# Kernel tuning notes

Hardware: AMD Instinct MI355X
Metric: run time of the kernel (lower is better)

The kernel has to match this reference:

```python
import jax, jax.numpy as jnp
import numpy as np

B, S, D = 2, 2048, 1024
H = 16            # attention heads
KVH = 4           # key/value heads
G = H // KVH      # group_size = 4
HD = D // H       # head_dim = 64
ROPE_THETA = 10000.0


def rope(x):
    # x: [B, S, D]; interleaved-pair rotary embedding over full last dim
    d = x.shape[-1]
    inv_freq = 1.0 / (ROPE_THETA ** (jnp.arange(0, d, 2, dtype=jnp.float32) / d))  # [d/2]
    ang = jnp.arange(x.shape[1], dtype=jnp.float32)[:, None] * inv_freq[None, :]   # [S, d/2]
    cos, sin = jnp.cos(ang), jnp.sin(ang)
    x1, x2 = x[..., 0::2], x[..., 1::2]
    r1 = x1 * cos - x2 * sin
    r2 = x1 * sin + x2 * cos
    out = jnp.stack([r1, r2], axis=-1).reshape(x.shape)
    return out


def setup_inputs() -> dict:
    key = jax.random.key(0)
    kx, kq, kk, kv = jax.random.split(key, 4)
    x = jax.random.normal(kx, (B, S, D), dtype=jnp.float32)
    # mark last 256 positions of batch element 1 as padding via NaN
    x = x.at[1, S - 256:, :].set(jnp.nan)
    scale = 1.0 / np.sqrt(D)
    Wq = jax.random.normal(kq, (D, D), dtype=jnp.float32) * scale
    Wk = jax.random.normal(kk, (D, D // G), dtype=jnp.float32) * scale
    Wv = jax.random.normal(kv, (D, D // G), dtype=jnp.float32) * scale
    return {"x": x, "Wq": Wq, "Wk": Wk, "Wv": Wv}


def reference(x, Wq, Wk, Wv):
    pad = jnp.isnan(x)                      # [B,S,D]
    x = jnp.where(pad, 0.0, x)
    key_pad = jnp.any(pad, axis=-1)         # [B,S] True = padded token

    q = x @ Wq                              # [B,S,D]
    k = jnp.repeat(x @ Wk, G, axis=-1)      # grouped KV, repeat_interleave -> [B,S,D]
    v = jnp.repeat(x @ Wv, G, axis=-1)

    q = rope(q)
    k = rope(k)

    def split_heads(t):
        return t.reshape(B, S, H, HD).transpose(0, 2, 1, 3)  # [B,H,S,HD]

    q, k, v = split_heads(q), split_heads(k), split_heads(v)

    scores = jnp.einsum('bhqd,bhkd->bhqk', q, k) / np.sqrt(HD)
    causal = jnp.tril(jnp.ones((S, S), dtype=bool))
    allow = causal[None, None, :, :] & (~key_pad)[:, None, None, :]
    scores = jnp.where(allow, scores, -1e9)
    attn = jax.nn.softmax(scores, axis=-1)
    out = jnp.einsum('bhqk,bhkd->bhqd', attn, v)
    return out.transpose(0, 2, 1, 3).reshape(B, S, D)
```

## Files before the change

kernel.cpp:

```cpp
#include <hip/hip_runtime.h>
#include <hip/hip_bf16.h>
#include <math.h>

typedef unsigned short u16;
typedef unsigned int u32;
typedef __bf16 bf16x8 __attribute__((ext_vector_type(8)));
typedef float fx4 __attribute__((ext_vector_type(4)));

#define MFMA16(a, b, c) __builtin_amdgcn_mfma_f32_16x16x32_bf16(a, b, c, 0, 0, 0)

static constexpr int Bb = 2, Ss = 2048, Dd = 1024, Hh = 16, DKV = 256;
static constexpr int NQKV = 1536;
static constexpr int ROWS = Bb * Ss;
static constexpr float L2T_OVER = 0.0259525632f;
static constexpr float SC2 = 0.18033688f;
static constexpr int PSTR = 76;
static constexpr int NUNITS = 2560;

__device__ __forceinline__ u16 f2bf(float f) {
    union { float f; u32 i; } v; v.f = f;
    u32 u = v.i;
    return (u16)((u + 0x7FFFu + ((u >> 16) & 1u)) >> 16);
}
__device__ __forceinline__ u16 bfr(float f) {
    return (u16)((__float_as_uint(f) + 0x8000u) >> 16);
}

__device__ __forceinline__ float fexp2(float x) {
    float r; asm("v_exp_f32 %0, %1" : "=v"(r) : "v"(x)); return r;
}
__device__ __forceinline__ void fsincos(float a, float& sn, float& cs) {
    float r = a * 0.15915494309189535f;
    r = r - floorf(r);
    asm("v_sin_f32 %0, %1" : "=v"(sn) : "v"(r));
    asm("v_cos_f32 %0, %1" : "=v"(cs) : "v"(r));
}

__device__ __forceinline__ void gl16(const u16* g, u16* l) {
    __builtin_amdgcn_global_load_lds(
        (const __attribute__((address_space(1))) void*)g,
        (__attribute__((address_space(3))) void*)l, 16, 0, 0);
}

template <int CTRL>
__device__ __forceinline__ float dppf(float x) {
    return __int_as_float(
        __builtin_amdgcn_mov_dpp(__float_as_int(x), CTRL, 0xF, 0xF, true));
}
__device__ __forceinline__ float rsum16(float x) {
    x += dppf<0xB1>(x);
    x += dppf<0x4E>(x);
    x += dppf<0x124>(x);
    x += dppf<0x128>(x);
    return x;
}

__global__ void pre_kernel(const float* __restrict__ x, const float* __restrict__ Wq,
                           const float* __restrict__ Wk, const float* __restrict__ Wv,
                           u16* __restrict__ xc, u32* __restrict__ kpb,
                           u16* __restrict__ wAll) {
    __shared__ u16 tile[32][33];
    __shared__ int flag;
    int bid = blockIdx.x, t = threadIdx.x;
    if (bid < 4096) {
        int row = bid;
        if (t == 0) flag = 0;
        __syncthreads();
        float4 d = *(const float4*)(x + (size_t)row * Dd + t * 4);
        int any = 0;
        float a0 = d.x, a1 = d.y, a2 = d.z, a3 = d.w;
        if ((__float_as_uint(a0) & 0x7FFFFFFFu) > 0x7F800000u) { a0 = 0.f; any = 1; }
        if ((__float_as_uint(a1) & 0x7FFFFFFFu) > 0x7F800000u) { a1 = 0.f; any = 1; }
        if ((__float_as_uint(a2) & 0x7FFFFFFFu) > 0x7F800000u) { a2 = 0.f; any = 1; }
        if ((__float_as_uint(a3) & 0x7FFFFFFFu) > 0x7F800000u) { a3 = 0.f; any = 1; }
        if (any) atomicOr(&flag, 1);
        uint2 o;
        o.x = (u32)f2bf(a0) | ((u32)f2bf(a1) << 16);
        o.y = (u32)f2bf(a2) | ((u32)f2bf(a3) << 16);
        *(uint2*)(xc + (size_t)row * Dd + t * 4) = o;
        __syncthreads();
        if (t == 0 && flag) {
            int b = row >> 11, s = row & (Ss - 1);
            atomicOr(&kpb[b * 64 + (s >> 5)], 1u << (s & 31));
        }
        return;
    }
    const float* in; u16* out; int C, bx, by;
    if (bid < 5120) { int i = bid - 4096; in = Wq; out = wAll; C = Dd; bx = i & 31; by = i >> 5; }
    else if (bid < 5376) { int i = bid - 5120; in = Wk; out = wAll + (size_t)Dd * Dd; C = DKV; bx = i & 7; by = i >> 3; }
    else { int i = bid - 5376; in = Wv; out = wAll + (size_t)1280 * Dd; C = DKV; bx = i & 7; by = i >> 3; }
    int c0 = bx * 32, r0 = by * 32;
    int tx = t & 31, ty = t >> 5;
    for (int i = 0; i < 32; i += 8)
        tile[ty + i][tx] = f2bf(in[(size_t)(r0 + ty + i) * C + c0 + tx]);
    __syncthreads();
    for (int i = 0; i < 32; i += 8)
        out[(size_t)(c0 + ty + i) * Dd + r0 + tx] = tile[tx][ty + i];
}

__global__ __launch_bounds__(256) void gemm_qkv(
    const u16* __restrict__ A, const u16* __restrict__ Bt, u16* __restrict__ C) {
    __shared__ __align__(16) u16 As[2][128 * 32];
    __shared__ __align__(16) u16 Bs[2][64 * 32];
    int t = threadIdx.x, w = t >> 6, lane = t & 63;
    int l15 = lane & 15, quad = lane >> 4;
    int col0 = blockIdx.x * 64, row0 = blockIdx.y * 128;
    int wm = w >> 1, wn = w & 1;
    fx4 acc[4][2];
#pragma unroll
    for (int i = 0; i < 4; ++i)
#pragma unroll
        for (int j = 0; j < 2; ++j) acc[i][j] = (fx4){0.f, 0.f, 0.f, 0.f};

    auto stage = [&](int kb, int buf) {
#pragma unroll
        for (int i = 0; i < 2; ++i) {
            int slot = i * 256 + t;
            int row = slot >> 2, p = slot & 3, g = p ^ ((row >> 1) & 3);
            gl16(A + (size_t)(row0 + row) * Dd + kb * 32 + g * 8,
                 &As[buf][(i * 256 + w * 64) * 8]);
        }
        {
            int row = t >> 2, p = t & 3, g = p ^ ((row >> 1) & 3);
            gl16(Bt + (size_t)(col0 + row) * Dd + kb * 32 + g * 8,
                 &Bs[buf][(w * 64) * 8]);
        }
    };

    stage(0, 0);
    int buf = 0;
    for (int kb = 0; kb < 32; ++kb) {
        __syncthreads();
        if (kb + 1 < 32) stage(kb + 1, buf ^ 1);
        bf16x8 af[4], bfr2[2];
#pragma unroll
        for (int mi = 0; mi < 4; ++mi) {
            int row = wm * 64 + mi * 16 + l15;
            af[mi] = *(const bf16x8*)(&As[buf][row * 32 + ((quad ^ ((row >> 1) & 3)) * 8)]);
        }
#pragma unroll
        for (int ni = 0; ni < 2; ++ni) {
            int row = wn * 32 + ni * 16 + l15;
            bfr2[ni] = *(const bf16x8*)(&Bs[buf][row * 32 + ((quad ^ ((row >> 1) & 3)) * 8)]);
        }
#pragma unroll
        for (int mi = 0; mi < 4; ++mi)
#pragma unroll
            for (int ni = 0; ni < 2; ++ni)
                acc[mi][ni] = MFMA16(af[mi], bfr2[ni], acc[mi][ni]);
        buf ^= 1;
    }
#pragma unroll
    for (int mi = 0; mi < 4; ++mi) {
        int rbase = row0 + wm * 64 + mi * 16 + quad * 4;
#pragma unroll
        for (int ni = 0; ni < 2; ++ni) {
            int ccol = col0 + wn * 32 + ni * 16 + l15;
#pragma unroll
            for (int r = 0; r < 4; ++r)
                C[(size_t)(rbase + r) * NQKV + ccol] = f2bf(acc[mi][ni][r]);
        }
    }
}

__global__ void post_kernel(const u16* __restrict__ qkv, u16* __restrict__ kr,
                            u16* __restrict__ vtb) {
    __shared__ u16 tile[32][33];
    int bid = blockIdx.x, t = threadIdx.x;
    if (bid < 4096) {
        int row = bid;
        float pos = (float)(row & (Ss - 1));
        float kv = __uint_as_float(((u32)qkv[(size_t)row * NQKV + Dd + t]) << 16);
        float j0 = (float)(2 * t), j1 = j0 + 1.0f;
        float f0 = fexp2(-j0 * L2T_OVER), f1 = fexp2(-j1 * L2T_OVER);
        float s0, c0, s1, c1;
        fsincos(pos * f0, s0, c0);
        fsincos(pos * f1, s1, c1);
        float r0 = kv * (c0 - s0), r1 = kv * (s0 + c0);
        float r2 = kv * (c1 - s1), r3 = kv * (s1 + c1);
        uint2 o;
        o.x = (u32)f2bf(r0) | ((u32)f2bf(r1) << 16);
        o.y = (u32)f2bf(r2) | ((u32)f2bf(r3) << 16);
        *(uint2*)(kr + (size_t)row * Dd + t * 4) = o;
        return;
    }
    int i = bid - 4096;
    int b = i >> 9, by = (i & 511) >> 3, bx = i & 7;
    int c0 = bx * 32, r0 = by * 32;
    int tx = t & 31, ty = t >> 5;
    for (int k = 0; k < 32; k += 8)
        tile[ty + k][tx] = qkv[(size_t)(b * Ss + r0 + ty + k) * NQKV + 1280 + c0 + tx];
    __syncthreads();
    for (int k = 0; k < 32; k += 8)
        vtb[(size_t)(b * DKV + c0 + ty + k) * Ss + r0 + tx] = tile[tx][ty + k];
}

__device__ __forceinline__ bf16x8 ropeFrag(uint4 raw, float pos, float jbase) {
    u32 W[4] = {raw.x, raw.y, raw.z, raw.w};
    union { u32 u[4]; bf16x8 v; } o;
#pragma unroll
    for (int c = 0; c < 4; ++c) {
        float x0 = __uint_as_float(W[c] << 16);
        float x1 = __uint_as_float(W[c] & 0xFFFF0000u);
        float f = fexp2(-(jbase + (float)c) * L2T_OVER);
        float sn, cs;
        fsincos(pos * f, sn, cs);
        float r0 = x0 * cs - x1 * sn, r1 = x0 * sn + x1 * cs;
        o.u[c] = (u32)f2bf(r0) | ((u32)f2bf(r1) << 16);
    }
    return o.v;
}

__global__ __launch_bounds__(256) void attn_kernel(
    const u16* __restrict__ qkv, const u16* __restrict__ kr,
    const u16* __restrict__ vt, const u32* __restrict__ kpb,
    u32* __restrict__ ctr, float* __restrict__ O16, float* __restrict__ Lsum) {
    __shared__ __align__(16) u16 Ks[2][64 * 64];
    __shared__ __align__(16) u16 Ps[4][16 * PSTR];
    __shared__ int s_unit;

    int t = threadIdx.x, w = t >> 6, lane = t & 63;
    int l15 = lane & 15, quad = lane >> 4;

    for (;;) {
        if (t == 0) s_unit = (int)atomicAdd(ctr, 1u);
        __syncthreads();
        int unit = s_unit;
        if (unit >= NUNITS) return;

        int u = unit >> 5, hh = unit & 31;
        int tile, c;
        if (u < 32)      { tile = 24 + (u & 7); c = u >> 3; }
        else if (u < 56) { tile = 16 + ((u - 32) & 7); c = (u - 32) >> 3; }
        else if (u < 72) { tile = 8 + ((u - 56) & 7); c = (u - 56) >> 3; }
        else             { tile = 7 - (u - 72); c = 0; }
        int b = hh >> 4, h = hh & 15;
        int n = tile + 1, C = (n + 7) >> 3;
        int kb0 = (u32)(n * c) / (u32)C;
        int kbe = (u32)(n * (c + 1)) / (u32)C;
        int q0 = tile * 64;

        int pos = q0 + w * 16 + l15;
        const u16* qp = qkv + (size_t)(b * Ss + pos) * NQKV + h * 64;
        float jb = (float)(h * 32 + quad * 4);
        bf16x8 qf0 = ropeFrag(*(const uint4*)(qp + quad * 8), (float)pos, jb);
        bf16x8 qf1 = ropeFrag(*(const uint4*)(qp + 32 + quad * 8), (float)pos, jb + 16.f);

        u32 pw_all = kpb[b * 64 + lane];

        const u16* vrow = vt + (size_t)(b * DKV + h * 16 + l15) * Ss;

        auto stageK = [&](int k0, int buf) {
#pragma unroll
            for (int i2 = 0; i2 < 2; ++i2) {
                int row = i2 * 32 + w * 8 + (lane >> 3);
                int gg = (lane & 7) ^ (row & 7);
                gl16(kr + (size_t)(b * Ss + k0 + row) * Dd + h * 64 + gg * 8,
                     &Ks[buf][(i2 * 32 + w * 8) * 64]);
            }
        };

        float l_lane[4] = {0.f, 0.f, 0.f, 0.f};
        fx4 oacc = (fx4){0.f, 0.f, 0.f, 0.f};

        stageK(kb0 * 64, 0);
        int buf = 0;
        const int qrb = q0 + w * 16 + quad * 4;
        const int qmin = q0 + w * 16;

        for (int kb = kb0; kb < kbe; ++kb) {
            int k0 = kb * 64;
            __syncthreads();
            if (kb + 1 < kbe) stageK(k0 + 64, buf ^ 1);

            bf16x8 vf0 = *(const bf16x8*)(vrow + k0 + quad * 8);
            bf16x8 vf1 = *(const bf16x8*)(vrow + k0 + 32 + quad * 8);

            fx4 s[4];
#pragma unroll
            for (int tt = 0; tt < 4; ++tt) {
                const u16* kb_ = &Ks[buf][(tt * 16 + l15) * 64];
                bf16x8 kf0 = *(const bf16x8*)(kb_ + ((quad ^ (l15 & 7)) * 8));
                bf16x8 kf1 = *(const bf16x8*)(kb_ + (((quad + 4) ^ (l15 & 7)) * 8));
                fx4 z = (fx4){0.f, 0.f, 0.f, 0.f};
                fx4 a = MFMA16(qf0, kf0, z);
                s[tt] = MFMA16(qf1, kf1, a);
            }

            u32 pw0 = (u32)__shfl((int)pw_all, 2 * kb, 64);
            u32 pw1 = (u32)__shfl((int)pw_all, 2 * kb + 1, 64);
            bool fast = (k0 + 63 <= qmin) & ((pw0 | pw1) == 0u);

            float e[4][4];
            if (fast) {
#pragma unroll
                for (int tt = 0; tt < 4; ++tt)
#pragma unroll
                    for (int r = 0; r < 4; ++r)
                        e[tt][r] = fexp2(fmaf(s[tt][r], SC2, -32.f));
            } else {
                u32 padb[4];
#pragma unroll
                for (int tt = 0; tt < 4; ++tt)
                    padb[tt] = ((tt & 2 ? pw1 : pw0) >> ((tt * 16 + l15) & 31)) & 1u;
#pragma unroll
                for (int r = 0; r < 4; ++r) {
                    int qq = qrb + r;
#pragma unroll
                    for (int tt = 0; tt < 4; ++tt) {
                        float ee = fexp2(fmaf(s[tt][r], SC2, -32.f));
                        e[tt][r] = (k0 + tt * 16 + l15 <= qq && !padb[tt]) ? ee : 0.f;
                    }
                }
            }

#pragma unroll
            for (int r = 0; r < 4; ++r) {
                l_lane[r] += (e[0][r] + e[1][r]) + (e[2][r] + e[3][r]);
                int prow = (quad * 4 + r) * PSTR + l15;
                Ps[w][prow + 0] = bfr(e[0][r]);
                Ps[w][prow + 16] = bfr(e[1][r]);
                Ps[w][prow + 32] = bfr(e[2][r]);
                Ps[w][prow + 48] = bfr(e[3][r]);
            }

            {
                bf16x8 pf0 = *(const bf16x8*)(&Ps[w][l15 * PSTR + quad * 8]);
                bf16x8 pf1 = *(const bf16x8*)(&Ps[w][l15 * PSTR + 32 + quad * 8]);
                oacc = MFMA16(pf0, vf0, oacc);
                oacc = MFMA16(pf1, vf1, oacc);
            }
            buf ^= 1;
        }

        size_t obase = (size_t)hh * Ss;
#pragma unroll
        for (int r = 0; r < 4; ++r) {
            float l_row = rsum16(l_lane[r]);
            int q = qrb + r;
            atomicAdd(&O16[(obase + q) * 16 + l15], oacc[r]);
            if (l15 == 0) atomicAdd(&Lsum[obase + q], l_row);
        }
    }
}

__global__ void norm_kernel(const float* __restrict__ O16, const float* __restrict__ Lsum,
                            float* __restrict__ out) {
    int idx = blockIdx.x * 256 + threadIdx.x;
    int d4 = idx & 255;
    int row = idx >> 8;
    int h = d4 >> 4, f = d4 & 15;
    int b = row >> 11, s = row & (Ss - 1);
    size_t o = (size_t)(b * 16 + h) * Ss + s;
    float a = O16[o * 16 + f] / Lsum[o];
    float4 o4 = {a, a, a, a};
    *(float4*)(out + (size_t)row * Dd + d4 * 4) = o4;
}

extern "C" void kernel_launch(void* const* d_in, const int* in_sizes, int n_in,
                              void* d_out, int out_size, void* d_ws, size_t ws_size,
                              hipStream_t stream) {
    const float* x = (const float*)d_in[0];
    const float* Wq = (const float*)d_in[1];
    const float* Wk = (const float*)d_in[2];
    const float* Wv = (const float*)d_in[3];
    float* out = (float*)d_out;

    char* ws = (char*)d_ws;
    const size_t SZ_XC = (size_t)ROWS * Dd * 2;
    const size_t SZ_KPB = 4096;
    const size_t SZ_WALL = (size_t)NQKV * Dd * 2;
    const size_t SZ_QKV = (size_t)ROWS * NQKV * 2;
    const size_t SZ_O16 = (size_t)32 * Ss * 16 * 4;
    const size_t SZ_L = (size_t)32 * Ss * 4;

    size_t off = 0;
    u16* xc = (u16*)(ws + off);
    u16* krope = (u16*)(ws + off); off += SZ_XC;
    u32* kpb = (u32*)(ws + off); off += SZ_KPB;
    u16* wAll = (u16*)(ws + off);
    u16* vtb = (u16*)(ws + off); off += SZ_WALL;
    u16* qkv = (u16*)(ws + off); off += SZ_QKV;
    float* O16 = (float*)(ws + off); off += SZ_O16;
    float* Ls = (float*)(ws + off); off += SZ_L;
    u32* ctr = kpb + 192;
    (void)ws_size; (void)in_sizes; (void)n_in; (void)out_size;

    hipMemsetAsync(kpb, 0, 1024, stream);
    hipMemsetAsync(O16, 0, SZ_O16 + SZ_L, stream);
    pre_kernel<<<5632, 256, 0, stream>>>(x, Wq, Wk, Wv, xc, kpb, wAll);
    gemm_qkv<<<dim3(NQKV / 64, ROWS / 128), 256, 0, stream>>>(xc, wAll, qkv);
    post_kernel<<<5120, 256, 0, stream>>>(qkv, krope, vtb);
    attn_kernel<<<1536, 256, 0, stream>>>(qkv, krope, vtb, kpb, ctr, O16, Ls);
    norm_kernel<<<4096, 256, 0, stream>>>(O16, Ls, out);
}
```

Before: 176.8 us.

## Fuse K RoPE into QKV GEMM epilogue and drop persistent attention scheduler

When the workspace is large enough, the QKV GEMM blocks that cover the K columns apply rotary embedding in their epilogue and write the expanded K directly. That removes the 4096 RoPE blocks from the post kernel and one round trip of K through memory. The attention kernel also drops its atomic work-counter loop and launches one block per work unit, with the short tiles now ordered ascending instead of descending. The fused path depends on ws_size; with a small workspace it falls back to the old RoPE blocks, and the static launch loses dynamic load balancing.

```diff
diff --git a/kernel.cpp b/kernel.cpp
--- a/kernel.cpp
+++ b/kernel.cpp
@@ -15,7 +15,6 @@
 static constexpr float L2T_OVER = 0.0259525632f;
 static constexpr float SC2 = 0.18033688f;
 static constexpr int PSTR = 76;
-static constexpr int NUNITS = 2560;
 
 __device__ __forceinline__ u16 f2bf(float f) {
     union { float f; u32 i; } v; v.f = f;
@@ -99,7 +98,8 @@
 }
 
 __global__ __launch_bounds__(256) void gemm_qkv(
-    const u16* __restrict__ A, const u16* __restrict__ Bt, u16* __restrict__ C) {
+    const u16* __restrict__ A, const u16* __restrict__ Bt, u16* __restrict__ C,
+    u16* __restrict__ kr, int fuseK) {
     __shared__ __align__(16) u16 As[2][128 * 32];
     __shared__ __align__(16) u16 Bs[2][64 * 32];
     int t = threadIdx.x, w = t >> 6, lane = t & 63;
@@ -150,6 +150,33 @@
                 acc[mi][ni] = MFMA16(af[mi], bfr2[ni], acc[mi][ni]);
         buf ^= 1;
     }
+
+    if (fuseK && col0 >= 1024 && col0 < 1280) {
+#pragma unroll
+        for (int mi = 0; mi < 4; ++mi) {
+            int rbase = row0 + wm * 64 + mi * 16 + quad * 4;
+#pragma unroll
+            for (int ni = 0; ni < 2; ++ni) {
+                int tt = col0 + wn * 32 + ni * 16 + l15 - 1024;
+                float f0 = fexp2(-(float)(2 * tt) * L2T_OVER);
+                float f1 = fexp2(-(float)(2 * tt + 1) * L2T_OVER);
+#pragma unroll
+                for (int r = 0; r < 4; ++r) {
+                    int row = rbase + r;
+                    float pos = (float)(row & (Ss - 1));
+                    float s0, c0, s1, c1;
+                    fsincos(pos * f0, s0, c0);
+                    fsincos(pos * f1, s1, c1);
+                    float kv = acc[mi][ni][r];
+                    uint2 o;
+                    o.x = (u32)f2bf(kv * (c0 - s0)) | ((u32)f2bf(kv * (s0 + c0)) << 16);
+                    o.y = (u32)f2bf(kv * (c1 - s1)) | ((u32)f2bf(kv * (s1 + c1)) << 16);
+                    *(uint2*)(kr + (size_t)row * Dd + 4 * tt) = o;
+                }
+            }
+        }
+        return;
+    }
 #pragma unroll
     for (int mi = 0; mi < 4; ++mi) {
         int rbase = row0 + wm * 64 + mi * 16 + quad * 4;
@@ -164,10 +191,10 @@
 }
 
 __global__ void post_kernel(const u16* __restrict__ qkv, u16* __restrict__ kr,
-                            u16* __restrict__ vtb) {
+                            u16* __restrict__ vtb, int ropeBlocks) {
     __shared__ u16 tile[32][33];
     int bid = blockIdx.x, t = threadIdx.x;
-    if (bid < 4096) {
+    if (bid < ropeBlocks) {
         int row = bid;
         float pos = (float)(row & (Ss - 1));
         float kv = __uint_as_float(((u32)qkv[(size_t)row * NQKV + Dd + t]) << 16);
@@ -184,7 +211,7 @@
         *(uint2*)(kr + (size_t)row * Dd + t * 4) = o;
         return;
     }
-    int i = bid - 4096;
+    int i = bid - ropeBlocks;
     int b = i >> 9, by = (i & 511) >> 3, bx = i & 7;
     int c0 = bx * 32, r0 = by * 32;
     int tx = t & 31, ty = t >> 5;
@@ -214,133 +241,125 @@
 __global__ __launch_bounds__(256) void attn_kernel(
     const u16* __restrict__ qkv, const u16* __restrict__ kr,
     const u16* __restrict__ vt, const u32* __restrict__ kpb,
-    u32* __restrict__ ctr, float* __restrict__ O16, float* __restrict__ Lsum) {
+    float* __restrict__ O16, float* __restrict__ Lsum) {
     __shared__ __align__(16) u16 Ks[2][64 * 64];
     __shared__ __align__(16) u16 Ps[4][16 * PSTR];
-    __shared__ int s_unit;
 
     int t = threadIdx.x, w = t >> 6, lane = t & 63;
     int l15 = lane & 15, quad = lane >> 4;
-
-    for (;;) {
-        if (t == 0) s_unit = (int)atomicAdd(ctr, 1u);
+    int bid = blockIdx.x;
+    int u = bid >> 5, hh = bid & 31;
+    int tile, c;
+    if (u < 32)      { tile = 24 + (u & 7); c = u >> 3; }
+    else if (u < 56) { tile = 16 + ((u - 32) & 7); c = (u - 32) >> 3; }
+    else if (u < 72) { tile = 8 + ((u - 56) & 7); c = (u - 56) >> 3; }
+    else             { tile = u - 72; c = 0; }
+    int b = hh >> 4, h = hh & 15;
+    int n = tile + 1, C = (n + 7) >> 3;
+    int kb0 = (int)((u32)(n * c) / (u32)C);
+    int kbe = (int)((u32)(n * (c + 1)) / (u32)C);
+    int q0 = tile * 64;
+
+    int pos = q0 + w * 16 + l15;
+    const u16* qp = qkv + (size_t)(b * Ss + pos) * NQKV + h * 64;
+    float jb = (float)(h * 32 + quad * 4);
+    bf16x8 qf0 = ropeFrag(*(const uint4*)(qp + quad * 8), (float)pos, jb);
+    bf16x8 qf1 = ropeFrag(*(const uint4*)(qp + 32 + quad * 8), (float)pos, jb + 16.f);
+
+    u32 pw_all = kpb[b * 64 + lane];
+
+    const u16* vrow = vt + (size_t)(b * DKV + h * 16 + l15) * Ss;
+
+    auto stageK = [&](int k0, int buf) {
+#pragma unroll
+        for (int i2 = 0; i2 < 2; ++i2) {
+            int row = i2 * 32 + w * 8 + (lane >> 3);
+            int gg = (lane & 7) ^ (row & 7);
+            gl16(kr + (size_t)(b * Ss + k0 + row) * Dd + h * 64 + gg * 8,
+                 &Ks[buf][(i2 * 32 + w * 8) * 64]);
+        }
+    };
+
+    float l_lane[4] = {0.f, 0.f, 0.f, 0.f};
+    fx4 oacc = (fx4){0.f, 0.f, 0.f, 0.f};
+
+    stageK(kb0 * 64, 0);
+    int buf = 0;
+    const int qrb = q0 + w * 16 + quad * 4;
+    const int qmin = q0 + w * 16;
+
+    for (int kb = kb0; kb < kbe; ++kb) {
+        int k0 = kb * 64;
         __syncthreads();
-        int unit = s_unit;
-        if (unit >= NUNITS) return;
-
-        int u = unit >> 5, hh = unit & 31;
-        int tile, c;
-        if (u < 32)      { tile = 24 + (u & 7); c = u >> 3; }
-        else if (u < 56) { tile = 16 + ((u - 32) & 7); c = (u - 32) >> 3; }
-        else if (u < 72) { tile = 8 + ((u - 56) & 7); c = (u - 56) >> 3; }
-        else             { tile = 7 - (u - 72); c = 0; }
-        int b = hh >> 4, h = hh & 15;
-        int n = tile + 1, C = (n + 7) >> 3;
-        int kb0 = (u32)(n * c) / (u32)C;
-        int kbe = (u32)(n * (c + 1)) / (u32)C;
-        int q0 = tile * 64;
-
-        int pos = q0 + w * 16 + l15;
-        const u16* qp = qkv + (size_t)(b * Ss + pos) * NQKV + h * 64;
-        float jb = (float)(h * 32 + quad * 4);
-        bf16x8 qf0 = ropeFrag(*(const uint4*)(qp + quad * 8), (float)pos, jb);
-        bf16x8 qf1 = ropeFrag(*(const uint4*)(qp + 32 + quad * 8), (float)pos, jb + 16.f);
-
-        u32 pw_all = kpb[b * 64 + lane];
-
-        const u16* vrow = vt + (size_t)(b * DKV + h * 16 + l15) * Ss;
-
-        auto stageK = [&](int k0, int buf) {
-#pragma unroll
-            for (int i2 = 0; i2 < 2; ++i2) {
-                int row = i2 * 32 + w * 8 + (lane >> 3);
-                int gg = (lane & 7) ^ (row & 7);
-                gl16(kr + (size_t)(b * Ss + k0 + row) * Dd + h * 64 + gg * 8,
-                     &Ks[buf][(i2 * 32 + w * 8) * 64]);
-            }
-        };
-
-        float l_lane[4] = {0.f, 0.f, 0.f, 0.f};
-        fx4 oacc = (fx4){0.f, 0.f, 0.f, 0.f};
-
-        stageK(kb0 * 64, 0);
-        int buf = 0;
-        const int qrb = q0 + w * 16 + quad * 4;
-        const int qmin = q0 + w * 16;
-
-        for (int kb = kb0; kb < kbe; ++kb) {
-            int k0 = kb * 64;
-            __syncthreads();
-            if (kb + 1 < kbe) stageK(k0 + 64, buf ^ 1);
-
-            bf16x8 vf0 = *(const bf16x8*)(vrow + k0 + quad * 8);
-            bf16x8 vf1 = *(const bf16x8*)(vrow + k0 + 32 + quad * 8);
-
-            fx4 s[4];
-#pragma unroll
-            for (int tt = 0; tt < 4; ++tt) {
-                const u16* kb_ = &Ks[buf][(tt * 16 + l15) * 64];
-                bf16x8 kf0 = *(const bf16x8*)(kb_ + ((quad ^ (l15 & 7)) * 8));
-                bf16x8 kf1 = *(const bf16x8*)(kb_ + (((quad + 4) ^ (l15 & 7)) * 8));
-                fx4 z = (fx4){0.f, 0.f, 0.f, 0.f};
-                fx4 a = MFMA16(qf0, kf0, z);
-                s[tt] = MFMA16(qf1, kf1, a);
-            }
-
-            u32 pw0 = (u32)__shfl((int)pw_all, 2 * kb, 64);
-            u32 pw1 = (u32)__shfl((int)pw_all, 2 * kb + 1, 64);
-            bool fast = (k0 + 63 <= qmin) & ((pw0 | pw1) == 0u);
-
-            float e[4][4];
-            if (fast) {
-#pragma unroll
-                for (int tt = 0; tt < 4; ++tt)
-#pragma unroll
-                    for (int r = 0; r < 4; ++r)
-                        e[tt][r] = fexp2(fmaf(s[tt][r], SC2, -32.f));
-            } else {
-                u32 padb[4];
-#pragma unroll
-                for (int tt = 0; tt < 4; ++tt)
-                    padb[tt] = ((tt & 2 ? pw1 : pw0) >> ((tt * 16 + l15) & 31)) & 1u;
-#pragma unroll
-                for (int r = 0; r < 4; ++r) {
-                    int qq = qrb + r;
-#pragma unroll
-                    for (int tt = 0; tt < 4; ++tt) {
-                        float ee = fexp2(fmaf(s[tt][r], SC2, -32.f));
-                        e[tt][r] = (k0 + tt * 16 + l15 <= qq && !padb[tt]) ? ee : 0.f;
-                    }
+        if (kb + 1 < kbe) stageK(k0 + 64, buf ^ 1);
+
+        bf16x8 vf0 = *(const bf16x8*)(vrow + k0 + quad * 8);
+        bf16x8 vf1 = *(const bf16x8*)(vrow + k0 + 32 + quad * 8);
+
+        fx4 s[4];
+#pragma unroll
+        for (int tt = 0; tt < 4; ++tt) {
+            const u16* kb_ = &Ks[buf][(tt * 16 + l15) * 64];
+            bf16x8 kf0 = *(const bf16x8*)(kb_ + ((quad ^ (l15 & 7)) * 8));
+            bf16x8 kf1 = *(const bf16x8*)(kb_ + (((quad + 4) ^ (l15 & 7)) * 8));
+            fx4 z = (fx4){0.f, 0.f, 0.f, 0.f};
+            fx4 a = MFMA16(qf0, kf0, z);
+            s[tt] = MFMA16(qf1, kf1, a);
+        }
+
+        u32 pw0 = (u32)__shfl((int)pw_all, 2 * kb, 64);
+        u32 pw1 = (u32)__shfl((int)pw_all, 2 * kb + 1, 64);
+        bool fast = (k0 + 63 <= qmin) & ((pw0 | pw1) == 0u);
+
+        float e[4][4];
+        if (fast) {
+#pragma unroll
+            for (int tt = 0; tt < 4; ++tt)
+#pragma unroll
+                for (int r = 0; r < 4; ++r)
+                    e[tt][r] = fexp2(fmaf(s[tt][r], SC2, -32.f));
+        } else {
+            u32 padb[4];
+#pragma unroll
+            for (int tt = 0; tt < 4; ++tt)
+                padb[tt] = ((tt & 2 ? pw1 : pw0) >> ((tt * 16 + l15) & 31)) & 1u;
+#pragma unroll
+            for (int r = 0; r < 4; ++r) {
+                int qq = qrb + r;
+#pragma unroll
+                for (int tt = 0; tt < 4; ++tt) {
+                    float ee = fexp2(fmaf(s[tt][r], SC2, -32.f));
+                    e[tt][r] = (k0 + tt * 16 + l15 <= qq && !padb[tt]) ? ee : 0.f;
                 }
             }
-
-#pragma unroll
-            for (int r = 0; r < 4; ++r) {
-                l_lane[r] += (e[0][r] + e[1][r]) + (e[2][r] + e[3][r]);
-                int prow = (quad * 4 + r) * PSTR + l15;
-                Ps[w][prow + 0] = bfr(e[0][r]);
-                Ps[w][prow + 16] = bfr(e[1][r]);
-                Ps[w][prow + 32] = bfr(e[2][r]);
-                Ps[w][prow + 48] = bfr(e[3][r]);
-            }
-
-            {
-                bf16x8 pf0 = *(const bf16x8*)(&Ps[w][l15 * PSTR + quad * 8]);
-                bf16x8 pf1 = *(const bf16x8*)(&Ps[w][l15 * PSTR + 32 + quad * 8]);
-                oacc = MFMA16(pf0, vf0, oacc);
-                oacc = MFMA16(pf1, vf1, oacc);
-            }
-            buf ^= 1;
-        }
-
-        size_t obase = (size_t)hh * Ss;
+        }
+
 #pragma unroll
         for (int r = 0; r < 4; ++r) {
-            float l_row = rsum16(l_lane[r]);
-            int q = qrb + r;
-            atomicAdd(&O16[(obase + q) * 16 + l15], oacc[r]);
-            if (l15 == 0) atomicAdd(&Lsum[obase + q], l_row);
-        }
+            l_lane[r] += (e[0][r] + e[1][r]) + (e[2][r] + e[3][r]);
+            int prow = (quad * 4 + r) * PSTR + l15;
+            Ps[w][prow + 0] = bfr(e[0][r]);
+            Ps[w][prow + 16] = bfr(e[1][r]);
+            Ps[w][prow + 32] = bfr(e[2][r]);
+            Ps[w][prow + 48] = bfr(e[3][r]);
+        }
+
+        {
+            bf16x8 pf0 = *(const bf16x8*)(&Ps[w][l15 * PSTR + quad * 8]);
+            bf16x8 pf1 = *(const bf16x8*)(&Ps[w][l15 * PSTR + 32 + quad * 8]);
+            oacc = MFMA16(pf0, vf0, oacc);
+            oacc = MFMA16(pf1, vf1, oacc);
+        }
+        buf ^= 1;
+    }
+
+    size_t obase = (size_t)hh * Ss;
+#pragma unroll
+    for (int r = 0; r < 4; ++r) {
+        float l_row = rsum16(l_lane[r]);
+        int q = qrb + r;
+        atomicAdd(&O16[(obase + q) * 16 + l15], oacc[r]);
+        if (l15 == 0) atomicAdd(&Lsum[obase + q], l_row);
     }
 }
 
@@ -373,24 +392,28 @@
     const size_t SZ_QKV = (size_t)ROWS * NQKV * 2;
     const size_t SZ_O16 = (size_t)32 * Ss * 16 * 4;
     const size_t SZ_L = (size_t)32 * Ss * 4;
+    const size_t SZ_KR = (size_t)ROWS * Dd * 2;
 
     size_t off = 0;
-    u16* xc = (u16*)(ws + off);
-    u16* krope = (u16*)(ws + off); off += SZ_XC;
+    u16* xc = (u16*)(ws + off); off += SZ_XC;
     u32* kpb = (u32*)(ws + off); off += SZ_KPB;
     u16* wAll = (u16*)(ws + off);
     u16* vtb = (u16*)(ws + off); off += SZ_WALL;
     u16* qkv = (u16*)(ws + off); off += SZ_QKV;
     float* O16 = (float*)(ws + off); off += SZ_O16;
     float* Ls = (float*)(ws + off); off += SZ_L;
-    u32* ctr = kpb + 192;
-    (void)ws_size; (void)in_sizes; (void)n_in; (void)out_size;
+
+    int fuseK = (ws_size >= off + SZ_KR) ? 1 : 0;
+    u16* krope = fuseK ? (u16*)(ws + off) : xc;
+
+    (void)in_sizes; (void)n_in; (void)out_size;
 
     hipMemsetAsync(kpb, 0, 1024, stream);
     hipMemsetAsync(O16, 0, SZ_O16 + SZ_L, stream);
     pre_kernel<<<5632, 256, 0, stream>>>(x, Wq, Wk, Wv, xc, kpb, wAll);
-    gemm_qkv<<<dim3(NQKV / 64, ROWS / 128), 256, 0, stream>>>(xc, wAll, qkv);
-    post_kernel<<<5120, 256, 0, stream>>>(qkv, krope, vtb);
-    attn_kernel<<<1536, 256, 0, stream>>>(qkv, krope, vtb, kpb, ctr, O16, Ls);
+    gemm_qkv<<<dim3(NQKV / 64, ROWS / 128), 256, 0, stream>>>(xc, wAll, qkv, krope, fuseK);
+    int ropeBlocks = fuseK ? 0 : 4096;
+    post_kernel<<<ropeBlocks + 1024, 256, 0, stream>>>(qkv, krope, vtb, ropeBlocks);
+    attn_kernel<<<2560, 256, 0, stream>>>(qkv, krope, vtb, kpb, O16, Ls);
     norm_kernel<<<4096, 256, 0, stream>>>(O16, Ls, out);
 }
```

After: 150.7 us. 1.17x faster.
